# Kernel tuning notes

Measured on AMD Instinct MI355X. Metric: run time of the kernel, lower is better.

Reference implementation:

```python
import jax, jax.numpy as jnp
import numpy as np

B, C, T, D = 16, 1024, 2048, 512
EPS = 1e-5


def setup_inputs() -> dict:
    key = jax.random.key(0)
    ks = jax.random.split(key, 11)
    s_c = 1.0 / np.sqrt(C)
    s_d = 1.0 / np.sqrt(D)
    return {
        "x": jax.random.normal(ks[0], (B, C, T), dtype=jnp.float32),
        "Wq": jax.random.uniform(ks[1], (D, C), jnp.float32, -s_c, s_c),
        "bq": jax.random.uniform(ks[2], (D,), jnp.float32, -s_c, s_c),
        "Wk": jax.random.uniform(ks[3], (D, C), jnp.float32, -s_c, s_c),
        "bk": jax.random.uniform(ks[4], (D,), jnp.float32, -s_c, s_c),
        "Wv": jax.random.uniform(ks[5], (D, C), jnp.float32, -s_c, s_c),
        "bv": jax.random.uniform(ks[6], (D,), jnp.float32, -s_c, s_c),
        "Wo": jax.random.uniform(ks[7], (C, D), jnp.float32, -s_d, s_d),
        "bo": jax.random.uniform(ks[8], (C,), jnp.float32, -s_d, s_d),
        "gamma": jax.random.normal(ks[9], (C,), dtype=jnp.float32) * 0.1,
        "beta": jax.random.normal(ks[10], (C,), dtype=jnp.float32) * 0.1,
    }


def reference(x, Wq, bq, Wk, bk, Wv, bv, Wo, bo, gamma, beta):
    b, c, t = x.shape
    d = Wq.shape[0]
    # 1x1 Conv1d projections == channel-wise GEMMs
    q = jnp.einsum('dc,bct->btd', Wq, x) + bq            # (B, T, D)
    k = jnp.einsum('dc,bct->bdt', Wk, x) + bk[None, :, None]  # (B, D, T)
    v = jnp.einsum('dc,bct->bdt', Wv, x) + bv[None, :, None]  # (B, D, T)
    # sub_sample: MaxPool1d(kernel=2) on key/value along time
    k = k.reshape(b, d, t // 2, 2).max(axis=-1)          # (B, D, S)
    v = v.reshape(b, d, t // 2, 2).max(axis=-1)          # (B, D, S)
    # softmax-free attention: (Q @ K) / T then @ V
    attn = jnp.einsum('btd,bds->bts', q, k) / t          # (B, T, S)
    out = jnp.einsum('bts,bds->bdt', attn, v)            # (B, D, T)
    # output 1x1 conv
    y = jnp.einsum('cd,bdt->bct', Wo, out) + bo[None, :, None]  # (B, C, T)
    # BatchNorm1d (training-mode batch stats, biased variance)
    mu = y.mean(axis=(0, 2), keepdims=True)
    var = y.var(axis=(0, 2), keepdims=True)
    y = gamma[None, :, None] * (y - mu) * jax.lax.rsqrt(var + EPS) + beta[None, :, None]
    return y + x
```

## Files before the change

### kernel.cpp

```cpp
#include <hip/hip_runtime.h>

typedef unsigned short ushort_t;
typedef __bf16 bf16x8 __attribute__((ext_vector_type(8)));
typedef float floatx4 __attribute__((ext_vector_type(4)));

__device__ __forceinline__ ushort_t f2bf(float f) {
  union { float f; unsigned int u; } c; c.f = f;
  unsigned int r = c.u + 0x7FFFu + ((c.u >> 16) & 1u);
  return (ushort_t)(r >> 16);
}

__device__ __forceinline__ void async16(const ushort_t* g, ushort_t* l) {
  __builtin_amdgcn_global_load_lds(
      (const __attribute__((address_space(1))) unsigned int*)g,
      (__attribute__((address_space(3))) unsigned int*)l, 16, 0, 0);
}

template<int BIASM, int POOLM, bool OUTF32>
__global__ __launch_bounds__(512, 2)
void gemm256(const ushort_t* __restrict__ A, long aStr,
             const ushort_t* __restrict__ B, long bStr,
             void* __restrict__ Cp, long cStr,
             int K, int lda, int ldb, int ldc,
             const float* __restrict__ bias, float scale)
{
  __shared__ ushort_t As[2][256][64];
  __shared__ ushort_t Bs[2][256][64];

  A += (long)blockIdx.z * aStr;
  B += (long)blockIdx.z * bStr;
  float* Cf = (float*)Cp + (OUTF32 ? (long)blockIdx.z * cStr : 0);
  ushort_t* Cb = (ushort_t*)Cp + (OUTF32 ? 0 : (long)blockIdx.z * cStr);
  const int m0 = blockIdx.y * 256;
  const int n0 = blockIdx.x * 256;
  const int tid = threadIdx.x;
  const int lane = tid & 63;
  const int wid = tid >> 6;
  const int wm = wid >> 2;
  const int wn = wid & 3;
  const int l15 = lane & 15;
  const int lq  = lane >> 4;

  const int srow = tid >> 3;
  const int scb  = (((tid & 7) ^ (srow & 7)) << 3);
  const int dcb  = (tid & 7) << 3;

  const ushort_t* gA = A + (long)(m0 + srow) * lda + scb;
  const ushort_t* gB = B + (long)(n0 + srow) * ldb + scb;

  const int pb0 = ((lq ^ (l15 & 7)) << 3);
  const int pb1 = (((4 | lq) ^ (l15 & 7)) << 3);

  floatx4 acc[8][4];
#pragma unroll
  for (int i = 0; i < 8; ++i)
#pragma unroll
    for (int j = 0; j < 4; ++j)
#pragma unroll
      for (int r = 0; r < 4; ++r) acc[i][j][r] = 0.0f;

  bf16x8 aA[4][2], bB0[2][2], bB1[2][2];

  const int NT = K >> 6;
  const int NI = NT >> 1;

#define STAGE_A(sl, hf, kt) do { \
    const ushort_t* _s = gA + (long)((hf) * 128) * lda + ((kt) << 6); \
    async16(_s,                  &As[sl][(hf)*128      + srow][dcb]); \
    async16(_s + (long)64 * lda, &As[sl][(hf)*128 + 64 + srow][dcb]); \
  } while (0)
#define STAGE_B(sl, hf, kt) do { \
    const ushort_t* _s = gB + (long)((hf) * 128) * ldb + ((kt) << 6); \
    async16(_s,                  &Bs[sl][(hf)*128      + srow][dcb]); \
    async16(_s + (long)64 * ldb, &Bs[sl][(hf)*128 + 64 + srow][dcb]); \
  } while (0)
#define LD_A(sl, mh) do { \
    _Pragma("unroll") for (int _i = 0; _i < 4; ++_i) { \
      const int _r = wm*128 + (mh)*64 + _i*16 + l15; \
      aA[_i][0] = *(const bf16x8*)&As[sl][_r][pb0]; \
      aA[_i][1] = *(const bf16x8*)&As[sl][_r][pb1]; } \
  } while (0)
#define LD_B(sl, nh, dst) do { \
    _Pragma("unroll") for (int _j = 0; _j < 2; ++_j) { \
      const int _r = wn*64 + (nh)*32 + _j*16 + l15; \
      dst[_j][0] = *(const bf16x8*)&Bs[sl][_r][pb0]; \
      dst[_j][1] = *(const bf16x8*)&Bs[sl][_r][pb1]; } \
  } while (0)
#define MMA(mh, nh, bfr) do { \
    __builtin_amdgcn_s_setprio(1); \
    _Pragma("unroll") for (int _i = 0; _i < 4; ++_i) \
    _Pragma("unroll") for (int _j = 0; _j < 2; ++_j) { \
      floatx4& _c = acc[(mh)*4 + _i][(nh)*2 + _j]; \
      _c = __builtin_amdgcn_mfma_f32_16x16x32_bf16(aA[_i][0], (bfr)[_j][0], _c, 0, 0, 0); \
      _c = __builtin_amdgcn_mfma_f32_16x16x32_bf16(aA[_i][1], (bfr)[_j][1], _c, 0, 0, 0); } \
    __builtin_amdgcn_s_setprio(0); \
  } while (0)
#define SBAR  __builtin_amdgcn_s_barrier()
#define LGKM0 asm volatile("s_waitcnt lgkmcnt(0)" ::: "memory")
#define VM4   asm volatile("s_waitcnt vmcnt(4)" ::: "memory")
#define VM0   asm volatile("s_waitcnt vmcnt(0)" ::: "memory")

  STAGE_A(0, 0, 0); STAGE_A(0, 1, 0); STAGE_B(0, 0, 0); STAGE_B(0, 1, 0);
  STAGE_A(1, 0, 1); STAGE_B(1, 1, 1);
  VM4; SBAR;

  for (int i = 0; i < NI - 1; ++i) {
    const int t1 = 2*i + 1, t2 = 2*i + 2, t3 = 2*i + 3;
    LD_A(0, 0); LD_B(0, 0, bB0); STAGE_A(1, 1, t1);
    SBAR; LGKM0; MMA(0, 0, bB0); SBAR;
    LD_B(0, 1, bB1); STAGE_B(1, 0, t1);
    SBAR; LGKM0; MMA(0, 1, bB1); SBAR;
    LD_A(0, 1); STAGE_A(0, 0, t2);
    SBAR; LGKM0; MMA(1, 1, bB1); SBAR;
    STAGE_B(0, 1, t2);
    SBAR; LGKM0; MMA(1, 0, bB0); VM4; SBAR;
    LD_A(1, 0); LD_B(1, 0, bB0); STAGE_A(0, 1, t2);
    SBAR; LGKM0; MMA(0, 0, bB0); SBAR;
    LD_B(1, 1, bB1); STAGE_B(0, 0, t2);
    SBAR; LGKM0; MMA(0, 1, bB1); SBAR;
    LD_A(1, 1); STAGE_A(1, 0, t3);
    SBAR; LGKM0; MMA(1, 1, bB1); SBAR;
    STAGE_B(1, 1, t3);
    SBAR; LGKM0; MMA(1, 0, bB0); VM4; SBAR;
  }
  {
    const int t1 = NT - 1;
    LD_A(0, 0); LD_B(0, 0, bB0); STAGE_A(1, 1, t1);
    SBAR; LGKM0; MMA(0, 0, bB0); SBAR;
    LD_B(0, 1, bB1); STAGE_B(1, 0, t1);
    SBAR; LGKM0; MMA(0, 1, bB1); SBAR;
    LD_A(0, 1);
    SBAR; LGKM0; MMA(1, 1, bB1); SBAR;
    SBAR; LGKM0; MMA(1, 0, bB0); VM0; SBAR;
    LD_A(1, 0); LD_B(1, 0, bB0);
    SBAR; LGKM0; MMA(0, 0, bB0); SBAR;
    LD_B(1, 1, bB1);
    SBAR; LGKM0; MMA(0, 1, bB1); SBAR;
    LD_A(1, 1);
    SBAR; LGKM0; MMA(1, 1, bB1); SBAR;
    LGKM0; MMA(1, 0, bB0);
  }
#undef STAGE_A
#undef STAGE_B
#undef LD_A
#undef LD_B
#undef MMA
#undef SBAR
#undef LGKM0
#undef VM4
#undef VM0

#pragma unroll
  for (int mi = 0; mi < 8; ++mi) {
    const int mbase = m0 + wm*128 + (mi >> 2)*64 + (mi & 3)*16 + lq*4;
#pragma unroll
    for (int nj = 0; nj < 4; ++nj) {
      const int n = n0 + wn*64 + (nj >> 1)*32 + (nj & 1)*16 + l15;
      float v[4];
#pragma unroll
      for (int r = 0; r < 4; ++r) {
        v[r] = acc[mi][nj][r] * scale;
        if (BIASM == 1) v[r] += bias[mbase + r];
      }
      if (BIASM == 2) {
        const float bn_ = bias[n];
#pragma unroll
        for (int r = 0; r < 4; ++r) v[r] += bn_;
      }
      if (POOLM == 0) {
#pragma unroll
        for (int r = 0; r < 4; ++r) {
          if (OUTF32) Cf[(long)(mbase + r) * ldc + n] = v[r];
          else        Cb[(long)(mbase + r) * ldc + n] = f2bf(v[r]);
        }
      } else if (POOLM == 1) {
#pragma unroll
        for (int r = 0; r < 4; ++r) {
          float o = __shfl_xor(v[r], 1);
          float w = fmaxf(v[r], o);
          if ((lane & 1) == 0) {
            if (OUTF32) Cf[(long)(mbase + r) * ldc + (n >> 1)] = w;
            else        Cb[(long)(mbase + r) * ldc + (n >> 1)] = f2bf(w);
          }
        }
      } else {
        float w0 = fmaxf(v[0], v[1]);
        float w1 = fmaxf(v[2], v[3]);
        const int mh = mbase >> 1;
        if (OUTF32) {
          Cf[(long)mh * ldc + n] = w0;
          Cf[(long)(mh + 1) * ldc + n] = w1;
        } else {
          Cb[(long)mh * ldc + n] = f2bf(w0);
          Cb[(long)(mh + 1) * ldc + n] = f2bf(w1);
        }
      }
    }
  }
}

__global__ __launch_bounds__(256)
void transpose_f32_bf16(const float* __restrict__ src, ushort_t* __restrict__ dst,
                        int Rr, int Cl)
{
  __shared__ ushort_t tile[32][33];
  const long boff = (long)blockIdx.z * Rr * Cl;
  const int tx = threadIdx.x & 31;
  const int ty = threadIdx.x >> 5;
  const int c0 = blockIdx.x * 32;
  const int r0 = blockIdx.y * 32;
#pragma unroll
  for (int i = 0; i < 4; ++i) {
    int r = ty + i * 8;
    tile[r][tx] = f2bf(src[boff + (long)(r0 + r) * Cl + c0 + tx]);
  }
  __syncthreads();
#pragma unroll
  for (int i = 0; i < 4; ++i) {
    int r = ty + i * 8;
    dst[boff + (long)(c0 + r) * Rr + r0 + tx] = tile[tx][r];
  }
}

__global__ __launch_bounds__(256)
void convert4(const float* __restrict__ a, const float* __restrict__ b,
              const float* __restrict__ c, const float* __restrict__ d,
              ushort_t* __restrict__ dst, int n)
{
  const float* srcs[4] = {a, b, c, d};
  const float* s = srcs[blockIdx.y];
  int i = blockIdx.x * 256 + threadIdx.x;
  if (i < n) dst[(long)blockIdx.y * n + i] = f2bf(s[i]);
}

__global__ __launch_bounds__(256)
void bn_stats(const float* __restrict__ y, float* __restrict__ stats)
{
  const int c = blockIdx.x;
  float s = 0.0f, s2 = 0.0f;
  for (int b = 0; b < 16; ++b) {
    const float* row = y + ((long)b * 1024 + c) * 2048;
    for (int t = threadIdx.x; t < 2048; t += 256) {
      float v = row[t];
      s += v; s2 += v * v;
    }
  }
#pragma unroll
  for (int o = 32; o > 0; o >>= 1) { s += __shfl_down(s, o); s2 += __shfl_down(s2, o); }
  __shared__ float red[8];
  const int lane = threadIdx.x & 63, w = threadIdx.x >> 6;
  if (lane == 0) { red[w] = s; red[4 + w] = s2; }
  __syncthreads();
  if (threadIdx.x == 0) {
    s = red[0] + red[1] + red[2] + red[3];
    s2 = red[4] + red[5] + red[6] + red[7];
    const float inv = 1.0f / (16.0f * 2048.0f);
    float mean = s * inv;
    float var = s2 * inv - mean * mean;
    stats[c * 2] = mean;
    stats[c * 2 + 1] = rsqrtf(var + 1e-5f);
  }
}

__global__ __launch_bounds__(256)
void bn_apply(float* __restrict__ y, const float* __restrict__ x,
              const float* __restrict__ stats, const float* __restrict__ gamma,
              const float* __restrict__ beta)
{
  const int bc = blockIdx.x;
  const int c = bc & 1023;
  const long off = (long)bc * 2048;
  const float mean = stats[c * 2], rstd = stats[c * 2 + 1];
  const float g = gamma[c] * rstd;
  const float bt = beta[c];
  for (int t = threadIdx.x; t < 2048; t += 256) {
    y[off + t] = (y[off + t] - mean) * g + bt + x[off + t];
  }
}

extern "C" void kernel_launch(void* const* d_in, const int* in_sizes, int n_in,
                              void* d_out, int out_size, void* d_ws, size_t ws_size,
                              hipStream_t stream) {
  (void)in_sizes; (void)n_in; (void)out_size; (void)ws_size;
  const float* x  = (const float*)d_in[0];
  const float* Wq = (const float*)d_in[1];
  const float* bq = (const float*)d_in[2];
  const float* Wk = (const float*)d_in[3];
  const float* bk = (const float*)d_in[4];
  const float* Wv = (const float*)d_in[5];
  const float* bv = (const float*)d_in[6];
  const float* Wo = (const float*)d_in[7];
  const float* bo = (const float*)d_in[8];
  const float* gamma = (const float*)d_in[9];
  const float* beta  = (const float*)d_in[10];
  float* out = (float*)d_out;

  const int Cc = 1024, T = 2048, D = 512, S = 1024;

  ushort_t* ws   = (ushort_t*)d_ws;
  ushort_t* xT   = ws;
  ushort_t* Qt   = ws + 33554432;
  ushort_t* Kt   = ws + 50331648;
  ushort_t* V    = ws + 58720256;
  ushort_t* attn = ws + 67108864;
  ushort_t* out2 = ws + 100663296;
  ushort_t* Wq_b = ws + 117440512;
  ushort_t* Wk_b = ws + 117964800;
  ushort_t* Wv_b = ws + 118489088;
  ushort_t* Wo_b = ws + 119013376;
  float*    stats = (float*)(ws + 119537664);

  dim3 blk(256);
  dim3 blk512(512);

  convert4<<<dim3(2048, 4), blk, 0, stream>>>(Wq, Wk, Wv, Wo, Wq_b, D * Cc);

  transpose_f32_bf16<<<dim3(T / 32, Cc / 32, 16), blk, 0, stream>>>(x, xT, Cc, T);

  gemm256<2, 0, false><<<dim3(D / 256, T / 256, 16), blk512, 0, stream>>>(
      xT, (long)T * Cc, Wq_b, 0, Qt, (long)T * D, Cc, Cc, Cc, D, bq, 1.0f);
  gemm256<2, 2, false><<<dim3(D / 256, T / 256, 16), blk512, 0, stream>>>(
      xT, (long)T * Cc, Wk_b, 0, Kt, (long)S * D, Cc, Cc, Cc, D, bk, 1.0f);
  gemm256<1, 1, false><<<dim3(T / 256, D / 256, 16), blk512, 0, stream>>>(
      Wv_b, 0, xT, (long)T * Cc, V, (long)D * S, Cc, Cc, Cc, S, bv, 1.0f);

  gemm256<0, 0, false><<<dim3(S / 256, T / 256, 16), blk512, 0, stream>>>(
      Qt, (long)T * D, Kt, (long)S * D, attn, (long)T * S,
      D, D, D, S, nullptr, 1.0f / 2048.0f);
  gemm256<0, 0, false><<<dim3(D / 256, T / 256, 16), blk512, 0, stream>>>(
      attn, (long)T * S, V, (long)D * S, out2, (long)T * D,
      S, S, S, D, nullptr, 1.0f);

  gemm256<1, 0, true><<<dim3(T / 256, Cc / 256, 16), blk512, 0, stream>>>(
      Wo_b, 0, out2, (long)T * D, out, (long)Cc * T, D, D, D, T, bo, 1.0f);

  bn_stats<<<dim3(1024), blk, 0, stream>>>(out, stats);
  bn_apply<<<dim3(16384), blk, 0, stream>>>(out, x, stats, gamma, beta);
}
```

Baseline: 616.7 us.

## Reassociate softmax-free attention as Q·(K·Vᵀ) and vectorize transpose/BN kernels

Since attention has no softmax, the product (Q·K)·V is reassociated to Q·(K·Vᵀ). A per-batch D×D matrix is computed from pooled K and V, then multiplied by Q, which avoids materializing the T×S attention matrix and cuts FLOPs for both attention GEMMs. K is now produced in the same D-major pooled layout as V. The x transpose uses 64×64 tiles with float4 loads and 16-byte stores, and the BN stats/apply kernels use float4 accesses. Rounding to bf16 now happens at a different intermediate (KVᵀ instead of attn), which slightly changes numerics.

```diff
diff --git a/kernel.cpp b/kernel.cpp
--- a/kernel.cpp
+++ b/kernel.cpp
@@ -3,6 +3,7 @@
 typedef unsigned short ushort_t;
 typedef __bf16 bf16x8 __attribute__((ext_vector_type(8)));
 typedef float floatx4 __attribute__((ext_vector_type(4)));
+typedef ushort_t ushortx8 __attribute__((ext_vector_type(8)));
 
 __device__ __forceinline__ ushort_t f2bf(float f) {
   union { float f; unsigned int u; } c; c.f = f;
@@ -203,22 +204,27 @@
 void transpose_f32_bf16(const float* __restrict__ src, ushort_t* __restrict__ dst,
                         int Rr, int Cl)
 {
-  __shared__ ushort_t tile[32][33];
+  __shared__ ushort_t tileT[64][72];
   const long boff = (long)blockIdx.z * Rr * Cl;
-  const int tx = threadIdx.x & 31;
-  const int ty = threadIdx.x >> 5;
-  const int c0 = blockIdx.x * 32;
-  const int r0 = blockIdx.y * 32;
+  const int t0 = blockIdx.x * 64;
+  const int r0 = blockIdx.y * 64;
+  const int tx = threadIdx.x & 15;
+  const int ty = threadIdx.x >> 4;
 #pragma unroll
   for (int i = 0; i < 4; ++i) {
-    int r = ty + i * 8;
-    tile[r][tx] = f2bf(src[boff + (long)(r0 + r) * Cl + c0 + tx]);
+    const int c = ty + 16 * i;
+    floatx4 v = *(const floatx4*)&src[boff + (long)(r0 + c) * Cl + t0 + 4 * tx];
+#pragma unroll
+    for (int j = 0; j < 4; ++j) tileT[4 * tx + j][c] = f2bf(v[j]);
   }
   __syncthreads();
-#pragma unroll
-  for (int i = 0; i < 4; ++i) {
-    int r = ty + i * 8;
-    dst[boff + (long)(c0 + r) * Rr + r0 + tx] = tile[tx][r];
+  const int cx = threadIdx.x & 7;
+  const int tw = threadIdx.x >> 3;
+#pragma unroll
+  for (int i = 0; i < 2; ++i) {
+    const int t = tw + 32 * i;
+    ushortx8 w = *(const ushortx8*)&tileT[t][8 * cx];
+    *(ushortx8*)&dst[boff + (long)(t0 + t) * Rr + r0 + 8 * cx] = w;
   }
 }
 
@@ -239,10 +245,11 @@
   const int c = blockIdx.x;
   float s = 0.0f, s2 = 0.0f;
   for (int b = 0; b < 16; ++b) {
-    const float* row = y + ((long)b * 1024 + c) * 2048;
-    for (int t = threadIdx.x; t < 2048; t += 256) {
-      float v = row[t];
-      s += v; s2 += v * v;
+    const floatx4* row = (const floatx4*)(y + ((long)b * 1024 + c) * 2048);
+    for (int t = threadIdx.x; t < 512; t += 256) {
+      floatx4 v = row[t];
+#pragma unroll
+      for (int r = 0; r < 4; ++r) { s += v[r]; s2 += v[r] * v[r]; }
     }
   }
 #pragma unroll
@@ -273,8 +280,14 @@
   const float mean = stats[c * 2], rstd = stats[c * 2 + 1];
   const float g = gamma[c] * rstd;
   const float bt = beta[c];
-  for (int t = threadIdx.x; t < 2048; t += 256) {
-    y[off + t] = (y[off + t] - mean) * g + bt + x[off + t];
+  floatx4* yp = (floatx4*)(y + off);
+  const floatx4* xp = (const floatx4*)(x + off);
+  for (int t = threadIdx.x; t < 512; t += 256) {
+    floatx4 v = yp[t];
+    floatx4 xv = xp[t];
+#pragma unroll
+    for (int r = 0; r < 4; ++r) v[r] = (v[r] - mean) * g + bt + xv[r];
+    yp[t] = v;
   }
 }
 
@@ -300,36 +313,36 @@
   ushort_t* ws   = (ushort_t*)d_ws;
   ushort_t* xT   = ws;
   ushort_t* Qt   = ws + 33554432;
-  ushort_t* Kt   = ws + 50331648;
+  ushort_t* Kd   = ws + 50331648;
   ushort_t* V    = ws + 58720256;
-  ushort_t* attn = ws + 67108864;
-  ushort_t* out2 = ws + 100663296;
-  ushort_t* Wq_b = ws + 117440512;
-  ushort_t* Wk_b = ws + 117964800;
-  ushort_t* Wv_b = ws + 118489088;
-  ushort_t* Wo_b = ws + 119013376;
-  float*    stats = (float*)(ws + 119537664);
+  ushort_t* Wt   = ws + 67108864;
+  ushort_t* out2 = ws + 71303168;
+  ushort_t* Wq_b = ws + 88080384;
+  ushort_t* Wk_b = ws + 88604672;
+  ushort_t* Wv_b = ws + 89128960;
+  ushort_t* Wo_b = ws + 89653248;
+  float*    stats = (float*)(ws + 90177536);
 
   dim3 blk(256);
   dim3 blk512(512);
 
   convert4<<<dim3(2048, 4), blk, 0, stream>>>(Wq, Wk, Wv, Wo, Wq_b, D * Cc);
 
-  transpose_f32_bf16<<<dim3(T / 32, Cc / 32, 16), blk, 0, stream>>>(x, xT, Cc, T);
+  transpose_f32_bf16<<<dim3(T / 64, Cc / 64, 16), blk, 0, stream>>>(x, xT, Cc, T);
 
   gemm256<2, 0, false><<<dim3(D / 256, T / 256, 16), blk512, 0, stream>>>(
       xT, (long)T * Cc, Wq_b, 0, Qt, (long)T * D, Cc, Cc, Cc, D, bq, 1.0f);
-  gemm256<2, 2, false><<<dim3(D / 256, T / 256, 16), blk512, 0, stream>>>(
-      xT, (long)T * Cc, Wk_b, 0, Kt, (long)S * D, Cc, Cc, Cc, D, bk, 1.0f);
+  gemm256<1, 1, false><<<dim3(T / 256, D / 256, 16), blk512, 0, stream>>>(
+      Wk_b, 0, xT, (long)T * Cc, Kd, (long)D * S, Cc, Cc, Cc, S, bk, 1.0f);
   gemm256<1, 1, false><<<dim3(T / 256, D / 256, 16), blk512, 0, stream>>>(
       Wv_b, 0, xT, (long)T * Cc, V, (long)D * S, Cc, Cc, Cc, S, bv, 1.0f);
 
-  gemm256<0, 0, false><<<dim3(S / 256, T / 256, 16), blk512, 0, stream>>>(
-      Qt, (long)T * D, Kt, (long)S * D, attn, (long)T * S,
-      D, D, D, S, nullptr, 1.0f / 2048.0f);
+  gemm256<0, 0, false><<<dim3(D / 256, D / 256, 16), blk512, 0, stream>>>(
+      V, (long)D * S, Kd, (long)D * S, Wt, (long)D * D,
+      S, S, S, D, nullptr, 1.0f);
   gemm256<0, 0, false><<<dim3(D / 256, T / 256, 16), blk512, 0, stream>>>(
-      attn, (long)T * S, V, (long)D * S, out2, (long)T * D,
-      S, S, S, D, nullptr, 1.0f);
+      Qt, (long)T * D, Wt, (long)D * D, out2, (long)T * D,
+      D, D, D, D, nullptr, 1.0f / 2048.0f);
 
   gemm256<1, 0, true><<<dim3(T / 256, Cc / 256, 16), blk512, 0, stream>>>(
       Wo_b, 0, out2, (long)T * D, out, (long)Cc * T, D, D, D, T, bo, 1.0f);
```

After: 554.0 us. 1.11x faster.
